# Performance work log

Measured on AMD Instinct MI355X. Metric: run time of the kernel, lower is better.

## Reference

```python
import jax, jax.numpy as jnp
import numpy as np

B, T, N = 2, 256, 512
H, S, C = 64, 8, 8
DYN = 4


def setup_inputs() -> dict:
    key = jax.random.key(0)
    ks = jax.random.split(key, 12)
    sc = 0.05
    return {
        "x": jax.random.normal(ks[0], (B, T, N), jnp.float32),
        "mask": (jax.random.uniform(ks[1], (B, T, N)) < 0.2).astype(jnp.float32),
        "static_context": jax.random.normal(ks[2], (N, S), jnp.float32),
        "node_coords": jax.random.normal(ks[3], (N, C), jnp.float32),
        "W1": jax.random.normal(ks[4], (DYN + S, H), jnp.float32) * sc,
        "b1": jnp.zeros((H,), jnp.float32),
        "W2": jax.random.normal(ks[5], (H, H), jnp.float32) * sc,
        "b2": jnp.zeros((H,), jnp.float32),
        "We1": jax.random.normal(ks[6], (4 * H, H), jnp.float32) * sc,
        "be1": jnp.zeros((H,), jnp.float32),
        "We2": jax.random.normal(ks[7], (H, 1), jnp.float32) * sc,
        "be2": jnp.zeros((1,), jnp.float32),
        "self_loop_logit": jnp.float32(0.5),
        "prior_strength": jnp.float32(1.0),
        "similarity_strength": jnp.float32(1.0),
        "temperature": jnp.float32(0.7),
    }


def reference(x, mask, static_context, node_coords, W1, b1, W2, b2,
              We1, be1, We2, be2, self_loop_logit, prior_strength,
              similarity_strength, temperature):
    Bv, Tv, Nv = x.shape
    # ---- dynamic per-node context over time ----
    observed = 1.0 - mask                                   # [B,T,N]
    count = jnp.maximum(observed.sum(axis=1), 1.0)          # [B,N]
    mean = (x * observed).sum(axis=1) / count               # [B,N]
    centered = (x - mean[:, None, :]) * observed
    std = jnp.sqrt((centered ** 2).sum(axis=1) / count + 1e-6)
    t_idx = jnp.arange(Tv, dtype=x.dtype)[None, :, None]
    latest = jnp.argmax(t_idx * observed, axis=1)           # [B,N] int
    last = jnp.take_along_axis(x, latest[:, None, :], axis=1)[:, 0, :]
    missing_ratio = mask.mean(axis=1)
    dyn = jnp.stack([mean, std, last, missing_ratio], axis=-1)  # [B,N,4]
    # ---- node encoder ----
    static = jnp.broadcast_to(static_context[None], (Bv, Nv, static_context.shape[-1]))
    feats = jnp.concatenate([dyn, static], axis=-1)
    h = jax.nn.relu(feats @ W1 + b1)
    h = jax.nn.relu(h @ W2 + b2)                            # [B,N,H]
    hn = h / jnp.maximum(jnp.linalg.norm(h, axis=-1, keepdims=True), 1e-12)
    # ---- edge MLP on pair features [h_i, h_j, |h_i-h_j|, h_i*h_j] ----
    # split first-layer weight into the four blocks so h_i/h_j terms are O(N)
    Wi, Wj, Wa, Wp = jnp.split(We1, 4, axis=0)              # each [H,H]
    pre_i = h @ Wi                                          # [B,N,H]
    pre_j = h @ Wj
    hi = h[:, :, None, :]                                   # [B,N,1,H]
    hj = h[:, None, :, :]                                   # [B,1,N,H]
    hidden = jax.nn.relu(pre_i[:, :, None, :] + pre_j[:, None, :, :]
                         + jnp.abs(hi - hj) @ Wa + (hi * hj) @ Wp + be1)
    edge_logits = (hidden @ We2 + be2)[..., 0]              # [B,N,N]
    # ---- cosine similarity + distance prior ----
    cos = jnp.einsum('bnh,bmh->bnm', hn, hn)
    eye = jnp.eye(Nv, dtype=x.dtype)
    off = 1.0 - eye
    diff = node_coords[:, None, :] - node_coords[None, :, :]
    dist = jnp.sqrt(jnp.maximum((diff ** 2).sum(-1), 1e-12))
    prior = (1.0 / (1.0 + dist)) * off                      # [N,N]
    # ---- combine, softmax, symmetrize, row-normalize ----
    logits = (edge_logits * off
              + jax.nn.softplus(prior_strength) * prior[None]
              + jax.nn.softplus(similarity_strength) * (cos * off))
    logits = logits + eye[None] * jax.nn.softplus(self_loop_logit)
    temp = jax.nn.softplus(temperature) + 1e-4
    adj = jax.nn.softmax(logits / temp, axis=-1)
    adj = 0.5 * (adj + jnp.swapaxes(adj, -1, -2))
    adj = adj / jnp.maximum(adj.sum(axis=-1, keepdims=True), 1e-6)
    return adj
```

## Files before the change

### kernel.cpp

```cpp
#include <hip/hip_runtime.h>
#include <hip/hip_bf16.h>
#include <math.h>

#define NB 2
#define NT 256
#define NN 512
#define NH 64
#define NS 8
#define NC 8

#define OFF_H      0
#define OFF_PVEC   65536
#define OFF_HF16   131072
#define OFF_HNF16  163840
#define OFF_WA16   196608
#define OFF_WJF    198656
#define OFF_WPF    202752
#define OFF_GEXT   206848
#define OFF_UNSYM  731136

typedef __attribute__((ext_vector_type(8))) _Float16 h8;
typedef __attribute__((ext_vector_type(2))) __fp16 fp16x2;
typedef __attribute__((ext_vector_type(4))) float f32x4;
typedef __attribute__((ext_vector_type(4))) unsigned u4;
typedef __attribute__((ext_vector_type(2))) unsigned u2;

__device__ __forceinline__ float softplusf(float x){
  if (x > 20.f) return x;
  return log1pf(expf(x));
}

__device__ __forceinline__ unsigned pkh(float a, float b){
  fp16x2 h = __builtin_amdgcn_cvt_pkrtz(a, b);
  return __builtin_bit_cast(unsigned, h);
}

template<int CTRL>
__device__ __forceinline__ float dpp_addf(float x){
  int xi = __builtin_bit_cast(int, x);
  int yi = __builtin_amdgcn_update_dpp(0, xi, CTRL, 0xF, 0xF, true);
  return x + __builtin_bit_cast(float, yi);
}
__device__ __forceinline__ float row16_sum(float x){
  x = dpp_addf<0xB1>(x);
  x = dpp_addf<0x4E>(x);
  x = dpp_addf<0x141>(x);
  x = dpp_addf<0x140>(x);
  return x;
}

__global__ __launch_bounds__(256) void k_front(
    const float* __restrict__ x, const float* __restrict__ mask,
    const float* __restrict__ sctx,
    const float* __restrict__ W1, const float* __restrict__ b1,
    const float* __restrict__ W2, const float* __restrict__ b2,
    const float* __restrict__ We1, const float* __restrict__ be1,
    float* __restrict__ hg, float* __restrict__ pvec,
    unsigned* __restrict__ hf16, unsigned* __restrict__ hn16,
    short* __restrict__ wa16, float* __restrict__ wjf,
    float* __restrict__ wpf){
  int blk = blockIdx.x;
  int tid = threadIdx.x;

  if (blk >= 256){
    int pidx = (blk - 256)*256 + tid;
    int e    = pidx & 7;
    int lane = (pidx >> 3) & 63;
    int frag = (pidx >> 9) & 7;
    int nt = frag & 3, ks = frag >> 2;
    int kg = lane >> 4, q = lane & 15;
    int kk = ks*32 + kg*8 + e;
    int c  = nt*16 + q;
    if (pidx < 4096){
      _Float16 v = (_Float16)We1[(128 + kk)*NH + c];
      wa16[pidx] = __builtin_bit_cast(short, v);
    } else if (pidx < 8192){
      wjf[pidx - 4096] = We1[(64 + kk)*NH + c];
    } else {
      wpf[pidx - 8192] = We1[(192 + kk)*NH + c];
    }
    return;
  }

  int b  = blk >> 7;
  int n0 = (blk & 127) * 4;

  int nl = tid & 3;
  int ts = tid >> 2;
  int n  = n0 + nl;

  float cnt = 0.f, sx = 0.f, sxx = 0.f;
  int lastt = 0;
  for (int t = ts*4; t < ts*4 + 4; ++t){
    int idx = (b*NT + t)*NN + n;
    float xv = x[idx];
    float mv = mask[idx];
    bool obs = (mv < 0.5f);
    if (obs){ cnt += 1.f; sx += xv; sxx += xv*xv; lastt = t; }
  }
  #pragma unroll
  for (int m = 4; m < 64; m <<= 1){
    cnt   += __shfl_xor(cnt,  m);
    sx    += __shfl_xor(sx,   m);
    sxx   += __shfl_xor(sxx,  m);
    lastt  = max(lastt, __shfl_xor(lastt, m));
  }
  int w = tid >> 6;
  __shared__ float r_cnt[4][4], r_sx[4][4], r_sxx[4][4];
  __shared__ int   r_lt[4][4];
  __shared__ float s_dyn[4][4];
  if ((tid & 63) < 4){
    r_cnt[w][nl] = cnt; r_sx[w][nl] = sx; r_sxx[w][nl] = sxx; r_lt[w][nl] = lastt;
  }
  __syncthreads();
  if (tid < 4){
    float c = 0.f, s1 = 0.f, s2 = 0.f; int lt = 0;
    #pragma unroll
    for (int ww = 0; ww < 4; ++ww){
      c  += r_cnt[ww][tid]; s1 += r_sx[ww][tid]; s2 += r_sxx[ww][tid];
      lt  = max(lt, r_lt[ww][tid]);
    }
    float cc   = fmaxf(c, 1.f);
    float mean = s1 / cc;
    float var  = s2 / cc - mean*mean;
    float stdv = sqrtf(fmaxf(var, 0.f) + 1e-6f);
    float last = x[(b*NT + lt)*NN + n0 + tid];
    float mr   = 1.f - c * (1.f/(float)NT);
    s_dyn[tid][0] = mean; s_dyn[tid][1] = stdv; s_dyn[tid][2] = last; s_dyn[tid][3] = mr;
  }
  __syncthreads();

  int c = tid & 63;
  int gn = n0 + w;
  int bn = b*NN + gn;
  __shared__ float s_f[4][12];
  __shared__ float s_h1[4][64];
  __shared__ float s_h2[4][64];

  if (c < 4)       s_f[w][c] = s_dyn[w][c];
  else if (c < 12) s_f[w][c] = sctx[gn*NS + (c-4)];
  __syncthreads();

  float a = b1[c];
  #pragma unroll
  for (int k = 0; k < 12; ++k) a = fmaf(s_f[w][k], W1[k*NH + c], a);
  s_h1[w][c] = fmaxf(a, 0.f);
  __syncthreads();

  float a2 = b2[c];
  #pragma unroll 8
  for (int k = 0; k < 64; ++k) a2 = fmaf(s_h1[w][k], W2[k*NH + c], a2);
  a2 = fmaxf(a2, 0.f);

  float sq = a2*a2;
  #pragma unroll
  for (int m = 1; m < 64; m <<= 1) sq += __shfl_xor(sq, m);
  float inv = 1.f / fmaxf(sqrtf(sq), 1e-12f);

  s_h2[w][c] = a2;
  __syncthreads();

  float pi = be1[c];
  #pragma unroll 8
  for (int k = 0; k < 64; ++k) pi = fmaf(s_h2[w][k], We1[k*NH + c], pi);

  hg  [bn*64 + c] = a2;
  pvec[bn*64 + c] = pi;
  if (c < 32){
    float e0 = s_h2[w][2*c], e1 = s_h2[w][2*c + 1];
    hf16[bn*32 + c] = pkh(e0, e1);
    hn16[bn*32 + c] = pkh(e0*inv, e1*inv);
  }
}

__global__ __launch_bounds__(256) void k_extra(
    const unsigned* __restrict__ hn16, const float* __restrict__ coords,
    const float* __restrict__ s_ss, const float* __restrict__ s_ps,
    const float* __restrict__ be2, float* __restrict__ gext){
  int b   = blockIdx.x;
  int i0  = blockIdx.y * 16;
  int jq  = blockIdx.z;
  int tid = threadIdx.x;
  int w   = tid >> 6;
  int lane = tid & 63;
  float spss = softplusf(s_ss[0]);
  float spps = softplusf(s_ps[0]);
  float be2v = be2[0];

  const u4* hv = (const u4*)hn16;
  int arow = i0 + (lane & 15);
  u4 a0 = hv[(b*NN + arow)*8 + (lane >> 4)];
  u4 a1 = hv[(b*NN + arow)*8 + (lane >> 4) + 4];
  h8 A0 = __builtin_bit_cast(h8, a0);
  h8 A1 = __builtin_bit_cast(h8, a1);

  #pragma unroll
  for (int t = 0; t < 2; ++t){
    int j0 = (jq*8 + w*2 + t) * 16;
    int jrow = j0 + (lane & 15);
    u4 b0 = hv[(b*NN + jrow)*8 + (lane >> 4)];
    u4 b1 = hv[(b*NN + jrow)*8 + (lane >> 4) + 4];
    f32x4 acc = (f32x4){0.f, 0.f, 0.f, 0.f};
    acc = __builtin_amdgcn_mfma_f32_16x16x32_f16(A0, __builtin_bit_cast(h8, b0), acc, 0, 0, 0);
    acc = __builtin_amdgcn_mfma_f32_16x16x32_f16(A1, __builtin_bit_cast(h8, b1), acc, 0, 0, 0);

    int jc = j0 + (lane & 15);
    float4 cj0 = *(const float4*)(coords + jc*NC);
    float4 cj1 = *(const float4*)(coords + jc*NC + 4);
    #pragma unroll
    for (int r = 0; r < 4; ++r){
      int irow = i0 + (lane >> 4)*4 + r;
      float4 ci0 = *(const float4*)(coords + irow*NC);
      float4 ci1 = *(const float4*)(coords + irow*NC + 4);
      float dd = 0.f;
      dd = fmaf(ci0.x-cj0.x, ci0.x-cj0.x, dd);
      dd = fmaf(ci0.y-cj0.y, ci0.y-cj0.y, dd);
      dd = fmaf(ci0.z-cj0.z, ci0.z-cj0.z, dd);
      dd = fmaf(ci0.w-cj0.w, ci0.w-cj0.w, dd);
      dd = fmaf(ci1.x-cj1.x, ci1.x-cj1.x, dd);
      dd = fmaf(ci1.y-cj1.y, ci1.y-cj1.y, dd);
      dd = fmaf(ci1.z-cj1.z, ci1.z-cj1.z, dd);
      dd = fmaf(ci1.w-cj1.w, ci1.w-cj1.w, dd);
      float dist  = sqrtf(fmaxf(dd, 1e-12f));
      float prior = (irow == jc) ? 0.f : spps / (1.f + dist);
      gext[(size_t)(b*NN + irow)*NN + jc] = fmaf(spss, acc[r], be2v + prior);
    }
  }
}

__global__ __launch_bounds__(512, 4) void k_logits(
    const float* __restrict__ hg, const float* __restrict__ pvec,
    const unsigned* __restrict__ hf16, const short* __restrict__ wa16,
    const float* __restrict__ wjf, const float* __restrict__ wpf,
    const float* __restrict__ We2, const float* __restrict__ gext,
    const float* __restrict__ s_sl, const float* __restrict__ s_tp,
    float* __restrict__ unsym){
  int blk = blockIdx.x;
  int b  = blk >> 8;
  int ip = (blk & 255) * 2;
  int tid  = threadIdx.x;
  int w    = tid >> 6;
  int lane = tid & 63;
  int q    = lane & 15;
  int kg   = lane >> 4;

  __shared__ __align__(16) float s_hi[2][64];
  __shared__ __align__(16) float s_ext[2][NN];
  __shared__ __align__(16) float lrow[2][NN];
  __shared__ __align__(16) unsigned lds_wa[2048];
  __shared__ __align__(16) unsigned lds_cw[2][2048];
  __shared__ __align__(16) unsigned s_hj[8][16*34 + 2];
  __shared__ float red[32];

  float spsl = softplusf(s_sl[0]);
  float invt = 1.f / (softplusf(s_tp[0]) + 1e-4f);

  if (tid < 128)
    s_hi[tid >> 6][tid & 63] = hg[(b*NN + ip + (tid >> 6))*64 + (tid & 63)];
  #pragma unroll
  for (int r = 0; r < 2; ++r)
    s_ext[r][tid] = gext[(size_t)(b*NN + ip + r)*NN + tid];
  __syncthreads();

  {
    int frag = tid >> 6;
    int l2   = tid & 63;
    const u4* wsrc = (const u4*)wa16;
    *(u4*)&lds_wa[(frag*64 + l2)*4] = wsrc[frag*64 + l2];

    int ch0 = (frag >> 2)*32 + (l2 >> 4)*8;
    const float* wj = wjf + (frag*64 + l2)*8;
    const float* wp = wpf + (frag*64 + l2)*8;
    #pragma unroll
    for (int r = 0; r < 2; ++r){
      u4 u;
      #pragma unroll
      for (int d = 0; d < 4; ++d){
        float v0 = fmaf(s_hi[r][ch0 + 2*d],     wp[2*d],     wj[2*d]);
        float v1 = fmaf(s_hi[r][ch0 + 2*d + 1], wp[2*d + 1], wj[2*d + 1]);
        u[d] = pkh(v0, v1);
      }
      *(u4*)&lds_cw[r][(frag*64 + l2)*4] = u;
    }
  }

  const u4* hfv = (const u4*)hf16;
  u4 hiA[2][2];
  #pragma unroll
  for (int r = 0; r < 2; ++r){
    hiA[r][0] = hfv[(b*NN + ip + r)*8 + kg];
    hiA[r][1] = hfv[(b*NN + ip + r)*8 + kg + 4];
  }

  float pv4[2][4], we2q[4];
  #pragma unroll
  for (int nt = 0; nt < 4; ++nt){
    #pragma unroll
    for (int r = 0; r < 2; ++r)
      pv4[r][nt] = pvec[(b*NN + ip + r)*64 + nt*16 + q];
    we2q[nt] = We2[nt*16 + q];
  }
  __syncthreads();

  unsigned* slice = &s_hj[w][0];
  const u4 absm = (u4){0x7fff7fffu, 0x7fff7fffu, 0x7fff7fffu, 0x7fff7fffu};

  #pragma unroll
  for (int s = 0; s < 4; ++s){
    int it = w + s*8;
    int jbase = it * 16;

    {
      int r8 = lane >> 3, c8 = lane & 7;
      u4 g0 = *(const u4*)((const unsigned*)hf16 + (size_t)(b*NN + jbase + r8)*32 + c8*4);
      u4 g1 = *(const u4*)((const unsigned*)hf16 + (size_t)(b*NN + jbase + 8 + r8)*32 + c8*4);
      unsigned* p0 = slice + r8*34 + c8*4;
      unsigned* p1 = slice + (8 + r8)*34 + c8*4;
      u2 t;
      t.x = g0.x; t.y = g0.y; *(u2*)p0 = t;
      t.x = g0.z; t.y = g0.w; *(u2*)(p0 + 2) = t;
      t.x = g1.x; t.y = g1.y; *(u2*)p1 = t;
      t.x = g1.z; t.y = g1.w; *(u2*)(p1 + 2) = t;
    }

    u4 hj0, hj1;
    {
      unsigned* rp = slice + q*34 + kg*4;
      u2 a0 = *(u2*)rp;
      u2 a1 = *(u2*)(rp + 2);
      u2 b0 = *(u2*)(rp + 16);
      u2 b1 = *(u2*)(rp + 18);
      hj0.x = a0.x; hj0.y = a0.y; hj0.z = a1.x; hj0.w = a1.y;
      hj1.x = b0.x; hj1.y = b0.y; hj1.z = b1.x; hj1.w = b1.y;
    }
    h8 hjv0 = __builtin_bit_cast(h8, hj0);
    h8 hjv1 = __builtin_bit_cast(h8, hj1);

    f32x4 acc[2][4];
    #pragma unroll
    for (int r = 0; r < 2; ++r)
      #pragma unroll
      for (int nt = 0; nt < 4; ++nt)
        acc[r][nt] = (f32x4){pv4[r][nt], pv4[r][nt], pv4[r][nt], pv4[r][nt]};

    #pragma unroll
    for (int nt = 0; nt < 4; ++nt){
      h8 wA0 = __builtin_bit_cast(h8, *(const u4*)&lds_wa[((0*4 + nt)*64 + lane)*4]);
      h8 wA1 = __builtin_bit_cast(h8, *(const u4*)&lds_wa[((1*4 + nt)*64 + lane)*4]);
      #pragma unroll
      for (int r = 0; r < 2; ++r){
        h8 dh0 = __builtin_bit_cast(h8, hiA[r][0]) - hjv0;
        h8 dh1 = __builtin_bit_cast(h8, hiA[r][1]) - hjv1;
        h8 af0 = __builtin_bit_cast(h8, __builtin_bit_cast(u4, dh0) & absm);
        h8 af1 = __builtin_bit_cast(h8, __builtin_bit_cast(u4, dh1) & absm);
        h8 wC0 = __builtin_bit_cast(h8, *(const u4*)&lds_cw[r][((0*4 + nt)*64 + lane)*4]);
        h8 wC1 = __builtin_bit_cast(h8, *(const u4*)&lds_cw[r][((1*4 + nt)*64 + lane)*4]);
        acc[r][nt] = __builtin_amdgcn_mfma_f32_16x16x32_f16(af0, wA0, acc[r][nt], 0, 0, 0);
        acc[r][nt] = __builtin_amdgcn_mfma_f32_16x16x32_f16(af1, wA1, acc[r][nt], 0, 0, 0);
        acc[r][nt] = __builtin_amdgcn_mfma_f32_16x16x32_f16(hjv0, wC0, acc[r][nt], 0, 0, 0);
        acc[r][nt] = __builtin_amdgcn_mfma_f32_16x16x32_f16(hjv1, wC1, acc[r][nt], 0, 0, 0);
      }
    }

    #pragma unroll
    for (int r = 0; r < 2; ++r){
      float part[4] = {0.f, 0.f, 0.f, 0.f};
      #pragma unroll
      for (int nt = 0; nt < 4; ++nt)
        #pragma unroll
        for (int rr = 0; rr < 4; ++rr)
          part[rr] = fmaf(fmaxf(acc[r][nt][rr], 0.f), we2q[nt], part[rr]);
      #pragma unroll
      for (int rr = 0; rr < 4; ++rr) part[rr] = row16_sum(part[rr]);

      if (q < 4){
        int j2 = jbase + kg*4 + q;
        float ps2 = part[0];
        ps2 = (q == 1) ? part[1] : ps2;
        ps2 = (q == 2) ? part[2] : ps2;
        ps2 = (q == 3) ? part[3] : ps2;
        float lg = ps2 + s_ext[r][j2];
        lrow[r][j2] = (j2 == ip + r) ? spsl : lg;
      }
    }
  }
  __syncthreads();

  float va = lrow[0][tid], vb = lrow[1][tid];
  float ma = va, mb = vb;
  #pragma unroll
  for (int msk = 1; msk < 64; msk <<= 1){
    ma = fmaxf(ma, __shfl_xor(ma, msk));
    mb = fmaxf(mb, __shfl_xor(mb, msk));
  }
  if (lane == 0){ red[w] = ma; red[8 + w] = mb; }
  __syncthreads();
  ma = red[0]; mb = red[8];
  #pragma unroll
  for (int ww = 1; ww < 8; ++ww){
    ma = fmaxf(ma, red[ww]);
    mb = fmaxf(mb, red[8 + ww]);
  }

  float ea = expf((va - ma) * invt);
  float eb = expf((vb - mb) * invt);
  float sa = ea, sb = eb;
  #pragma unroll
  for (int msk = 1; msk < 64; msk <<= 1){
    sa += __shfl_xor(sa, msk);
    sb += __shfl_xor(sb, msk);
  }
  if (lane == 0){ red[16 + w] = sa; red[24 + w] = sb; }
  __syncthreads();
  sa = red[16]; sb = red[24];
  #pragma unroll
  for (int ww = 1; ww < 8; ++ww){
    sa += red[16 + ww];
    sb += red[24 + ww];
  }

  unsym[(size_t)(b*NN + ip)*NN + tid]       = ea / sa;
  unsym[(size_t)(b*NN + ip + 1)*NN + tid]   = eb / sb;
}

__global__ __launch_bounds__(256) void k_sym(
    const float* __restrict__ u, float* __restrict__ out){
  int blk = blockIdx.x;
  int b = blk >> 9, i = blk & (NN-1);
  int tid = threadIdx.x;
  const float* urow = u + (size_t)(b*NN + i) * NN;
  float v0, v1, rs;
  {
    int j0 = tid, j1 = tid + 256;
    float a1 = urow[j0];
    float a2 = u[(size_t)(b*NN + j0) * NN + i];
    v0 = 0.5f*(a1 + a2);
    float a3 = urow[j1];
    float a4 = u[(size_t)(b*NN + j1) * NN + i];
    v1 = 0.5f*(a3 + a4);
    rs = v0 + v1;
  }
  int lane = tid & 63, w = tid >> 6;
  #pragma unroll
  for (int msk = 1; msk < 64; msk <<= 1) rs += __shfl_xor(rs, msk);
  __shared__ float red[4];
  if (lane == 0) red[w] = rs;
  __syncthreads();
  rs = red[0] + red[1] + red[2] + red[3];
  float inv = 1.f / fmaxf(rs, 1e-6f);
  float* orow = out + (size_t)(b*NN + i) * NN;
  orow[tid]       = v0 * inv;
  orow[tid + 256] = v1 * inv;
}

extern "C" void kernel_launch(void* const* d_in, const int* in_sizes, int n_in,
                              void* d_out, int out_size, void* d_ws, size_t ws_size,
                              hipStream_t stream){
  const float* x      = (const float*)d_in[0];
  const float* mask   = (const float*)d_in[1];
  const float* sctx   = (const float*)d_in[2];
  const float* coords = (const float*)d_in[3];
  const float* W1     = (const float*)d_in[4];
  const float* b1     = (const float*)d_in[5];
  const float* W2     = (const float*)d_in[6];
  const float* b2     = (const float*)d_in[7];
  const float* We1    = (const float*)d_in[8];
  const float* be1    = (const float*)d_in[9];
  const float* We2    = (const float*)d_in[10];
  const float* be2    = (const float*)d_in[11];
  const float* sl     = (const float*)d_in[12];
  const float* ps     = (const float*)d_in[13];
  const float* ss     = (const float*)d_in[14];
  const float* tp     = (const float*)d_in[15];

  float*    ws    = (float*)d_ws;
  float*    hgp   = ws + OFF_H;
  float*    pvecp = ws + OFF_PVEC;
  unsigned* hf16p = (unsigned*)(ws + OFF_HF16);
  unsigned* hn16p = (unsigned*)(ws + OFF_HNF16);
  short*    wa16p = (short*)(ws + OFF_WA16);
  float*    wjfp  = ws + OFF_WJF;
  float*    wpfp  = ws + OFF_WPF;
  float*    gext  = ws + OFF_GEXT;
  float*    unsym = ws + OFF_UNSYM;
  float*    out   = (float*)d_out;

  k_front <<<304, 256, 0, stream>>>(x, mask, sctx, W1, b1, W2, b2, We1, be1,
                                    hgp, pvecp, hf16p, hn16p, wa16p, wjfp, wpfp);
  k_extra <<<dim3(NB, 32, 4), 256, 0, stream>>>(hn16p, coords, ss, ps, be2, gext);
  k_logits<<<NB*NN/2, 512, 0, stream>>>(hgp, pvecp, hf16p, wa16p, wjfp, wpfp,
                                        We2, gext, sl, tp, unsym);
  k_sym   <<<NB*NN, 256, 0, stream>>>(unsym, out);
}
```

Baseline: 43.61 us.

## Switch edge MLP to 32x32x16 MFMA with shared hj panel staging

Rewrites the edge-MLP inner loop of the logits kernel to use 32x32x16 f16 MFMA tiles instead of 16x16x32, with the We1 weight pre-layout in the front kernel changed to match. The j-node features are staged into a block-wide 256-row LDS panel in two phases instead of per-wave 16-row slices, and the gext row is read directly at softmax time instead of being staged in LDS. The larger MFMA tile is meant to raise operand reuse and cut per-wave instruction and LDS overhead, at the cost of more accumulator registers. Occupancy bounds drop from 4 to 2 blocks per SM, and an extra barrier is added between the two panel phases.

```diff
diff --git a/kernel.cpp b/kernel.cpp
--- a/kernel.cpp
+++ b/kernel.cpp
@@ -19,11 +19,11 @@
 #define OFF_GEXT   206848
 #define OFF_UNSYM  731136
 
-typedef __attribute__((ext_vector_type(8))) _Float16 h8;
-typedef __attribute__((ext_vector_type(2))) __fp16 fp16x2;
-typedef __attribute__((ext_vector_type(4))) float f32x4;
-typedef __attribute__((ext_vector_type(4))) unsigned u4;
-typedef __attribute__((ext_vector_type(2))) unsigned u2;
+typedef __attribute__((ext_vector_type(8)))  _Float16 h8;
+typedef __attribute__((ext_vector_type(2)))  __fp16   fp16x2;
+typedef __attribute__((ext_vector_type(4)))  float    f32x4;
+typedef __attribute__((ext_vector_type(16))) float    f32x16;
+typedef __attribute__((ext_vector_type(4)))  unsigned u4;
 
 __device__ __forceinline__ float softplusf(float x){
   if (x > 20.f) return x;
@@ -67,17 +67,16 @@
     int e    = pidx & 7;
     int lane = (pidx >> 3) & 63;
     int frag = (pidx >> 9) & 7;
-    int nt = frag & 3, ks = frag >> 2;
-    int kg = lane >> 4, q = lane & 15;
-    int kk = ks*32 + kg*8 + e;
-    int c  = nt*16 + q;
+    int nh = frag & 1, s = frag >> 1;
+    int k  = s*16 + (lane >> 5)*8 + e;
+    int n  = nh*32 + (lane & 31);
     if (pidx < 4096){
-      _Float16 v = (_Float16)We1[(128 + kk)*NH + c];
+      _Float16 v = (_Float16)We1[(128 + k)*NH + n];
       wa16[pidx] = __builtin_bit_cast(short, v);
     } else if (pidx < 8192){
-      wjf[pidx - 4096] = We1[(64 + kk)*NH + c];
+      wjf[pidx - 4096] = We1[(64 + k)*NH + n];
     } else {
-      wpf[pidx - 8192] = We1[(192 + kk)*NH + c];
+      wpf[pidx - 8192] = We1[(192 + k)*NH + n];
     }
     return;
   }
@@ -228,7 +227,7 @@
   }
 }
 
-__global__ __launch_bounds__(512, 4) void k_logits(
+__global__ __launch_bounds__(512, 2) void k_logits(
     const float* __restrict__ hg, const float* __restrict__ pvec,
     const unsigned* __restrict__ hf16, const short* __restrict__ wa16,
     const float* __restrict__ wjf, const float* __restrict__ wpf,
@@ -241,34 +240,40 @@
   int tid  = threadIdx.x;
   int w    = tid >> 6;
   int lane = tid & 63;
-  int q    = lane & 15;
-  int kg   = lane >> 4;
-
-  __shared__ __align__(16) float s_hi[2][64];
-  __shared__ __align__(16) float s_ext[2][NN];
-  __shared__ __align__(16) float lrow[2][NN];
+  int jl   = lane & 31;
+  int kh   = lane >> 5;
+
+  __shared__ __align__(16) unsigned panel[256*34];
   __shared__ __align__(16) unsigned lds_wa[2048];
   __shared__ __align__(16) unsigned lds_cw[2][2048];
-  __shared__ __align__(16) unsigned s_hj[8][16*34 + 2];
-  __shared__ float red[32];
+  __shared__ __align__(16) float lrow[2][NN];
+  __shared__ __align__(16) float s_hi[2][64];
+  float* red = (float*)panel;
 
   float spsl = softplusf(s_sl[0]);
   float invt = 1.f / (softplusf(s_tp[0]) + 1e-4f);
 
   if (tid < 128)
     s_hi[tid >> 6][tid & 63] = hg[(b*NN + ip + (tid >> 6))*64 + (tid & 63)];
-  #pragma unroll
-  for (int r = 0; r < 2; ++r)
-    s_ext[r][tid] = gext[(size_t)(b*NN + ip + r)*NN + tid];
+
+  {
+    int row = tid >> 1, half = tid & 1;
+    const u4* src = (const u4*)(hf16 + (size_t)(b*NN + row)*32 + half*16);
+    unsigned* dst = panel + row*34 + half*16;
+    u4 v0 = src[0], v1 = src[1], v2 = src[2], v3 = src[3];
+    *(u4*)(dst)      = v0;
+    *(u4*)(dst + 4)  = v1;
+    *(u4*)(dst + 8)  = v2;
+    *(u4*)(dst + 12) = v3;
+  }
   __syncthreads();
 
   {
     int frag = tid >> 6;
     int l2   = tid & 63;
-    const u4* wsrc = (const u4*)wa16;
-    *(u4*)&lds_wa[(frag*64 + l2)*4] = wsrc[frag*64 + l2];
-
-    int ch0 = (frag >> 2)*32 + (l2 >> 4)*8;
+    *(u4*)&lds_wa[(frag*64 + l2)*4] = ((const u4*)wa16)[frag*64 + l2];
+
+    int cb = (frag >> 1)*16 + (l2 >> 5)*8;
     const float* wj = wjf + (frag*64 + l2)*8;
     const float* wp = wpf + (frag*64 + l2)*8;
     #pragma unroll
@@ -276,117 +281,111 @@
       u4 u;
       #pragma unroll
       for (int d = 0; d < 4; ++d){
-        float v0 = fmaf(s_hi[r][ch0 + 2*d],     wp[2*d],     wj[2*d]);
-        float v1 = fmaf(s_hi[r][ch0 + 2*d + 1], wp[2*d + 1], wj[2*d + 1]);
+        float v0 = fmaf(s_hi[r][cb + 2*d],     wp[2*d],     wj[2*d]);
+        float v1 = fmaf(s_hi[r][cb + 2*d + 1], wp[2*d + 1], wj[2*d + 1]);
         u[d] = pkh(v0, v1);
       }
       *(u4*)&lds_cw[r][(frag*64 + l2)*4] = u;
     }
   }
 
-  const u4* hfv = (const u4*)hf16;
-  u4 hiA[2][2];
-  #pragma unroll
-  for (int r = 0; r < 2; ++r){
-    hiA[r][0] = hfv[(b*NN + ip + r)*8 + kg];
-    hiA[r][1] = hfv[(b*NN + ip + r)*8 + kg + 4];
-  }
-
-  float pv4[2][4], we2q[4];
-  #pragma unroll
-  for (int nt = 0; nt < 4; ++nt){
+  u4 hiF[2][4];
+  #pragma unroll
+  for (int r = 0; r < 2; ++r)
+    #pragma unroll
+    for (int s = 0; s < 4; ++s)
+      hiF[r][s] = *(const u4*)(hf16 + (size_t)(b*NN + ip + r)*32 + s*8 + kh*4);
+
+  float pvv[2][2], we2v[2];
+  #pragma unroll
+  for (int nh = 0; nh < 2; ++nh){
     #pragma unroll
     for (int r = 0; r < 2; ++r)
-      pv4[r][nt] = pvec[(b*NN + ip + r)*64 + nt*16 + q];
-    we2q[nt] = We2[nt*16 + q];
-  }
-  __syncthreads();
-
-  unsigned* slice = &s_hj[w][0];
+      pvv[r][nh] = pvec[(b*NN + ip + r)*64 + nh*32 + jl];
+    we2v[nh] = We2[nh*32 + jl];
+  }
+  __syncthreads();
+
   const u4 absm = (u4){0x7fff7fffu, 0x7fff7fffu, 0x7fff7fffu, 0x7fff7fffu};
 
   #pragma unroll
-  for (int s = 0; s < 4; ++s){
-    int it = w + s*8;
-    int jbase = it * 16;
-
-    {
-      int r8 = lane >> 3, c8 = lane & 7;
-      u4 g0 = *(const u4*)((const unsigned*)hf16 + (size_t)(b*NN + jbase + r8)*32 + c8*4);
-      u4 g1 = *(const u4*)((const unsigned*)hf16 + (size_t)(b*NN + jbase + 8 + r8)*32 + c8*4);
-      unsigned* p0 = slice + r8*34 + c8*4;
-      unsigned* p1 = slice + (8 + r8)*34 + c8*4;
-      u2 t;
-      t.x = g0.x; t.y = g0.y; *(u2*)p0 = t;
-      t.x = g0.z; t.y = g0.w; *(u2*)(p0 + 2) = t;
-      t.x = g1.x; t.y = g1.y; *(u2*)p1 = t;
-      t.x = g1.z; t.y = g1.w; *(u2*)(p1 + 2) = t;
-    }
-
-    u4 hj0, hj1;
-    {
-      unsigned* rp = slice + q*34 + kg*4;
-      u2 a0 = *(u2*)rp;
-      u2 a1 = *(u2*)(rp + 2);
-      u2 b0 = *(u2*)(rp + 16);
-      u2 b1 = *(u2*)(rp + 18);
-      hj0.x = a0.x; hj0.y = a0.y; hj0.z = a1.x; hj0.w = a1.y;
-      hj1.x = b0.x; hj1.y = b0.y; hj1.z = b1.x; hj1.w = b1.y;
-    }
-    h8 hjv0 = __builtin_bit_cast(h8, hj0);
-    h8 hjv1 = __builtin_bit_cast(h8, hj1);
-
-    f32x4 acc[2][4];
+  for (int phase = 0; phase < 2; ++phase){
+    if (phase == 1){
+      __syncthreads();
+      int row = tid >> 1, half = tid & 1;
+      const u4* src = (const u4*)(hf16 + (size_t)(b*NN + 256 + row)*32 + half*16);
+      unsigned* dst = panel + row*34 + half*16;
+      u4 v0 = src[0], v1 = src[1], v2 = src[2], v3 = src[3];
+      *(u4*)(dst)      = v0;
+      *(u4*)(dst + 4)  = v1;
+      *(u4*)(dst + 8)  = v2;
+      *(u4*)(dst + 12) = v3;
+      __syncthreads();
+    }
+    int jbase = (w + phase*8) * 32;
+    int lr    = w*32 + jl;
+
+    u4 hjF[4];
+    const unsigned* prow = panel + lr*34 + kh*4;
+    #pragma unroll
+    for (int s = 0; s < 4; ++s) hjF[s] = *(const u4*)(prow + s*8);
+
+    f32x16 acc[2][2];
     #pragma unroll
     for (int r = 0; r < 2; ++r)
       #pragma unroll
-      for (int nt = 0; nt < 4; ++nt)
-        acc[r][nt] = (f32x4){pv4[r][nt], pv4[r][nt], pv4[r][nt], pv4[r][nt]};
-
-    #pragma unroll
-    for (int nt = 0; nt < 4; ++nt){
-      h8 wA0 = __builtin_bit_cast(h8, *(const u4*)&lds_wa[((0*4 + nt)*64 + lane)*4]);
-      h8 wA1 = __builtin_bit_cast(h8, *(const u4*)&lds_wa[((1*4 + nt)*64 + lane)*4]);
+      for (int nh = 0; nh < 2; ++nh)
+        #pragma unroll
+        for (int e = 0; e < 16; ++e) acc[r][nh][e] = pvv[r][nh];
+
+    #pragma unroll
+    for (int s = 0; s < 4; ++s){
+      h8 hjv = __builtin_bit_cast(h8, hjF[s]);
+      h8 wA0 = __builtin_bit_cast(h8, *(const u4*)&lds_wa[((s*2 + 0)*64 + lane)*4]);
+      h8 wA1 = __builtin_bit_cast(h8, *(const u4*)&lds_wa[((s*2 + 1)*64 + lane)*4]);
       #pragma unroll
       for (int r = 0; r < 2; ++r){
-        h8 dh0 = __builtin_bit_cast(h8, hiA[r][0]) - hjv0;
-        h8 dh1 = __builtin_bit_cast(h8, hiA[r][1]) - hjv1;
-        h8 af0 = __builtin_bit_cast(h8, __builtin_bit_cast(u4, dh0) & absm);
-        h8 af1 = __builtin_bit_cast(h8, __builtin_bit_cast(u4, dh1) & absm);
-        h8 wC0 = __builtin_bit_cast(h8, *(const u4*)&lds_cw[r][((0*4 + nt)*64 + lane)*4]);
-        h8 wC1 = __builtin_bit_cast(h8, *(const u4*)&lds_cw[r][((1*4 + nt)*64 + lane)*4]);
-        acc[r][nt] = __builtin_amdgcn_mfma_f32_16x16x32_f16(af0, wA0, acc[r][nt], 0, 0, 0);
-        acc[r][nt] = __builtin_amdgcn_mfma_f32_16x16x32_f16(af1, wA1, acc[r][nt], 0, 0, 0);
-        acc[r][nt] = __builtin_amdgcn_mfma_f32_16x16x32_f16(hjv0, wC0, acc[r][nt], 0, 0, 0);
-        acc[r][nt] = __builtin_amdgcn_mfma_f32_16x16x32_f16(hjv1, wC1, acc[r][nt], 0, 0, 0);
+        h8 dh = __builtin_bit_cast(h8, hiF[r][s]) - hjv;
+        h8 ad = __builtin_bit_cast(h8, __builtin_bit_cast(u4, dh) & absm);
+        h8 wC0 = __builtin_bit_cast(h8, *(const u4*)&lds_cw[r][((s*2 + 0)*64 + lane)*4]);
+        h8 wC1 = __builtin_bit_cast(h8, *(const u4*)&lds_cw[r][((s*2 + 1)*64 + lane)*4]);
+        acc[r][0] = __builtin_amdgcn_mfma_f32_32x32x16_f16(ad,  wA0, acc[r][0], 0, 0, 0);
+        acc[r][1] = __builtin_amdgcn_mfma_f32_32x32x16_f16(ad,  wA1, acc[r][1], 0, 0, 0);
+        acc[r][0] = __builtin_amdgcn_mfma_f32_32x32x16_f16(hjv, wC0, acc[r][0], 0, 0, 0);
+        acc[r][1] = __builtin_amdgcn_mfma_f32_32x32x16_f16(hjv, wC1, acc[r][1], 0, 0, 0);
       }
     }
 
     #pragma unroll
     for (int r = 0; r < 2; ++r){
-      float part[4] = {0.f, 0.f, 0.f, 0.f};
-      #pragma unroll
-      for (int nt = 0; nt < 4; ++nt)
-        #pragma unroll
-        for (int rr = 0; rr < 4; ++rr)
-          part[rr] = fmaf(fmaxf(acc[r][nt][rr], 0.f), we2q[nt], part[rr]);
-      #pragma unroll
-      for (int rr = 0; rr < 4; ++rr) part[rr] = row16_sum(part[rr]);
-
-      if (q < 4){
-        int j2 = jbase + kg*4 + q;
-        float ps2 = part[0];
-        ps2 = (q == 1) ? part[1] : ps2;
-        ps2 = (q == 2) ? part[2] : ps2;
-        ps2 = (q == 3) ? part[3] : ps2;
-        float lg = ps2 + s_ext[r][j2];
-        lrow[r][j2] = (j2 == ip + r) ? spsl : lg;
+      float t[16];
+      #pragma unroll
+      for (int reg = 0; reg < 16; ++reg){
+        float t0 = fmaxf(acc[r][0][reg], 0.f) * we2v[0];
+        t[reg] = fmaf(fmaxf(acc[r][1][reg], 0.f), we2v[1], t0);
       }
-    }
-  }
-  __syncthreads();
-
-  float va = lrow[0][tid], vb = lrow[1][tid];
+      #pragma unroll
+      for (int reg = 0; reg < 16; ++reg){
+        t[reg] = row16_sum(t[reg]);
+        t[reg] += __shfl_xor(t[reg], 16);
+      }
+      float sel = t[0];
+      #pragma unroll
+      for (int reg = 1; reg < 16; ++reg) sel = ((lane & 15) == reg) ? t[reg] : sel;
+      if ((lane & 31) < 16){
+        int rr = lane & 15;
+        int j2 = jbase + (rr & 3) + 8*(rr >> 2) + 4*kh;
+        lrow[r][j2] = sel;
+      }
+    }
+  }
+  __syncthreads();
+
+  float ga = gext[(size_t)(b*NN + ip)*NN + tid];
+  float gb = gext[(size_t)(b*NN + ip + 1)*NN + tid];
+  float va = (tid == ip)     ? spsl : lrow[0][tid] + ga;
+  float vb = (tid == ip + 1) ? spsl : lrow[1][tid] + gb;
+
   float ma = va, mb = vb;
   #pragma unroll
   for (int msk = 1; msk < 64; msk <<= 1){
@@ -419,8 +418,8 @@
     sb += red[24 + ww];
   }
 
-  unsym[(size_t)(b*NN + ip)*NN + tid]       = ea / sa;
-  unsym[(size_t)(b*NN + ip + 1)*NN + tid]   = eb / sb;
+  unsym[(size_t)(b*NN + ip)*NN + tid]     = ea / sa;
+  unsym[(size_t)(b*NN + ip + 1)*NN + tid] = eb / sb;
 }
 
 __global__ __launch_bounds__(256) void k_sym(
```

Measured after the change: 53.98 us. +23.8%, slower.
